# Kernel tuning notes

Measured on AMD Instinct MI355X. Metric: run time of the kernel, lower is better.

## Reference

```python
import jax, jax.numpy as jnp
import numpy as np

N = 400000       # maxvar(100000) * batch_size(4) nodes
E = 6400000      # edges, avg degree 16
D_IN, H, OUT = 1, 128, 2
N_MP = 4         # num_layers - 1 message-passing layers


def _bn(x, g, b):
    # BatchNorm1d in training mode: biased variance over the node/batch dim
    m = jnp.mean(x, axis=0)
    v = jnp.var(x, axis=0)
    return (x - m) * jax.lax.rsqrt(v + 1e-5) * g + b


def _gin_layer(h, src, dst, eps_l, W1, b1, g1, bb1, W2, b2, og, ob):
    # pooled = A @ h  (unweighted sparse adjacency) + (1+eps)*h
    pooled = jax.ops.segment_sum(h[src], dst, num_segments=N)
    pooled = pooled + (1.0 + eps_l) * h
    # 2-layer MLP (Linear -> BN -> ReLU -> Linear), then outer BN + ReLU
    x = jax.nn.relu(_bn(pooled @ W1 + b1, g1, bb1))
    x = x @ W2 + b2
    return jax.nn.relu(_bn(x, og, ob))


def setup_inputs() -> dict:
    key = jax.random.key(0)
    ks = jax.random.split(key, 10)
    f32 = jnp.float32
    inp = {
        "batch_size": 4,
        "var_feat": jax.random.normal(ks[0], (N, D_IN), f32),
        "edge_src": jax.random.randint(ks[1], (E,), 0, N, jnp.int32),
        "edge_dst": jax.random.randint(ks[2], (E,), 0, N, jnp.int32),
        "eps": jnp.ones((N_MP,), f32),
        # layer 0 MLP: D_IN -> H -> H
        "mlp0_W1": jax.random.normal(ks[3], (D_IN, H), f32) * 0.1,
        "mlp0_b1": jnp.zeros((H,), f32),
        "mlp0_g1": jnp.ones((H,), f32),
        "mlp0_bb1": jnp.zeros((H,), f32),
        "mlp0_W2": jax.random.normal(ks[4], (H, H), f32) * 0.05,
        "mlp0_b2": jnp.zeros((H,), f32),
        "bn0_g": jnp.ones((H,), f32),
        "bn0_b": jnp.zeros((H,), f32),
        # layers 1..3 MLPs stacked: H -> H -> H
        "mlpW1": jax.random.normal(ks[5], (N_MP - 1, H, H), f32) * 0.05,
        "mlpb1": jnp.zeros((N_MP - 1, H), f32),
        "mlpg1": jnp.ones((N_MP - 1, H), f32),
        "mlpbb1": jnp.zeros((N_MP - 1, H), f32),
        "mlpW2": jax.random.normal(ks[6], (N_MP - 1, H, H), f32) * 0.05,
        "mlpb2": jnp.zeros((N_MP - 1, H), f32),
        "bn_g": jnp.ones((N_MP - 1, H), f32),
        "bn_b": jnp.zeros((N_MP - 1, H), f32),
        # final classifier fc1: H -> OUT
        "fc1_W": jax.random.normal(ks[7], (H, OUT), f32) * 0.05,
        "fc1_b": jnp.zeros((OUT,), f32),
    }
    return inp


def reference(batch_size, var_feat, edge_src, edge_dst, eps,
              mlp0_W1, mlp0_b1, mlp0_g1, mlp0_bb1, mlp0_W2, mlp0_b2,
              bn0_g, bn0_b,
              mlpW1, mlpb1, mlpg1, mlpbb1, mlpW2, mlpb2, bn_g, bn_b,
              fc1_W, fc1_b):
    del batch_size  # unused in the var.var / no-lfa path
    h = _gin_layer(var_feat, edge_src, edge_dst, eps[0],
                   mlp0_W1, mlp0_b1, mlp0_g1, mlp0_bb1, mlp0_W2, mlp0_b2,
                   bn0_g, bn0_b)
    for l in range(N_MP - 1):
        h = _gin_layer(h, edge_src, edge_dst, eps[l + 1],
                       mlpW1[l], mlpb1[l], mlpg1[l], mlpbb1[l],
                       mlpW2[l], mlpb2[l], bn_g[l], bn_b[l])
    # var_classification head
    return jax.nn.softmax(h @ fc1_W + fc1_b, axis=1)
```

## Files before the change

### kernel.cpp

```cpp
#include <hip/hip_runtime.h>
#include <math.h>

#define HD 128
#define LDP 136

typedef _Float16 f16;
typedef _Float16 f16x8 __attribute__((ext_vector_type(8)));
typedef float f32x4 __attribute__((ext_vector_type(4)));

static __device__ __forceinline__ float h2f(unsigned short s) {
    f16 v; __builtin_memcpy(&v, &s, 2); return (float)v;
}

__global__ void k_diag(float* __restrict__ out, int n, float val) {
    for (int i = blockIdx.x * blockDim.x + threadIdx.x; i < n; i += gridDim.x * blockDim.x)
        out[i] = val;
}

__global__ void k_zero(float* __restrict__ p, int n) {
    for (int i = threadIdx.x; i < n; i += blockDim.x) p[i] = 0.f;
}
__global__ void k_zeroi(int* __restrict__ p, int n) {
    for (int i = blockIdx.x * blockDim.x + threadIdx.x; i < n; i += gridDim.x * blockDim.x)
        p[i] = 0;
}
__global__ void k_copyi(const int* __restrict__ a, int* __restrict__ b, int n) {
    for (int i = blockIdx.x * blockDim.x + threadIdx.x; i < n; i += gridDim.x * blockDim.x)
        b[i] = a[i];
}

__global__ void k_hist(const int* __restrict__ dst, int* __restrict__ row_ptr, int e) {
    for (int i = blockIdx.x * blockDim.x + threadIdx.x; i < e; i += gridDim.x * blockDim.x)
        atomicAdd(&row_ptr[dst[i] + 1], 1);
}

#define SCAN_B 1024
__global__ void k_scan_block(int* __restrict__ a, int n, int* __restrict__ bsum) {
    __shared__ int s[SCAN_B];
    int base = blockIdx.x * SCAN_B;
    int i = base + threadIdx.x;
    int v = (i < n) ? a[i] : 0;
    s[threadIdx.x] = v;
    __syncthreads();
    for (int o = 1; o < SCAN_B; o <<= 1) {
        int t = (threadIdx.x >= o) ? s[threadIdx.x - o] : 0;
        __syncthreads();
        s[threadIdx.x] += t;
        __syncthreads();
    }
    if (i < n) a[i] = s[threadIdx.x];
    if (threadIdx.x == 0) bsum[blockIdx.x] = s[SCAN_B - 1];
}
__global__ void k_scan_serial(int* __restrict__ bsum, int nb) {
    int run = 0;
    for (int b = 0; b < nb; b++) { int t = bsum[b]; bsum[b] = run; run += t; }
}
__global__ void k_scan_add(int* __restrict__ a, int n, const int* __restrict__ bsum) {
    int base = blockIdx.x * SCAN_B;
    int i = base + threadIdx.x;
    if (i < n) a[i] += bsum[blockIdx.x];
}
__global__ void k_bucket(const int* __restrict__ src, const int* __restrict__ dst,
                         int* __restrict__ fill, int* __restrict__ src_sorted, int e) {
    for (int i = blockIdx.x * blockDim.x + threadIdx.x; i < e; i += gridDim.x * blockDim.x) {
        int pos = atomicAdd(&fill[dst[i]], 1);
        src_sorted[pos] = src[i];
    }
}

__global__ void k_pool0(const float* __restrict__ vf, const int* __restrict__ row_ptr,
                        const int* __restrict__ srcs, const float* __restrict__ eps,
                        float* __restrict__ p0, int n) {
    float ep = 1.f + eps[0];
    for (int i = blockIdx.x * blockDim.x + threadIdx.x; i < n; i += gridDim.x * blockDim.x) {
        float s = ep * vf[i];
        int j1 = row_ptr[i + 1];
        for (int j = row_ptr[i]; j < j1; j++) s += vf[srcs[j]];
        p0[i] = s;
    }
}

__global__ void k_p0_stats(const float* __restrict__ p0, float* __restrict__ stats, int n) {
    __shared__ float rs[256], rq[256];
    float s = 0.f, q = 0.f;
    for (int i = blockIdx.x * blockDim.x + threadIdx.x; i < n; i += gridDim.x * blockDim.x) {
        float v = p0[i]; s += v; q += v * v;
    }
    int t = threadIdx.x;
    rs[t] = s; rq[t] = q;
    __syncthreads();
    for (int o = 128; o > 0; o >>= 1) {
        if (t < o) { rs[t] += rs[t + o]; rq[t] += rq[t + o]; }
        __syncthreads();
    }
    if (t == 0) { unsafeAtomicAdd(&stats[0], rs[0]); unsafeAtomicAdd(&stats[1], rq[0]); }
}

__global__ void k_l0_prep(float* __restrict__ stats, const float* __restrict__ W1,
                          const float* __restrict__ g1, const float* __restrict__ bb1,
                          float* __restrict__ A0, float* __restrict__ Sh0, int n) {
    float mp = stats[0] / n;
    float vp = stats[1] / n - mp * mp;
    int c = threadIdx.x;
    float w = W1[c];
    A0[c] = w * rsqrtf(vp * w * w + 1e-5f) * g1[c];
    Sh0[c] = bb1[c];
    if (c == 0) stats[2] = mp;
}

static __device__ __forceinline__ void acc_aff(f16x8 v, const float* scv, const float* shv,
                                               float* a) {
#pragma unroll
    for (int j = 0; j < 8; j++)
        a[j] += fmaxf((float)v[j] * scv[j] + shv[j], 0.f);
}

__global__ __launch_bounds__(256) void k_pgemm(
    const f16* __restrict__ h, const int* __restrict__ row_ptr,
    const int* __restrict__ src_sorted, const float* __restrict__ eps, int li,
    const float* __restrict__ sc, const float* __restrict__ sh,
    const float* __restrict__ W, const float* __restrict__ bias,
    f16* __restrict__ out, float* __restrict__ gsum, float* __restrict__ gsq, int n) {
    __shared__ f16 Wl[HD * LDP];
    __shared__ f16 Pl[32 * LDP];
    const int t = threadIdx.x;
    const int lane = t & 63, w = t >> 6;
    const int l15 = lane & 15, lq = lane >> 4;

    for (int p = 0; p < 64; p++) {
        int idx = p * 256 + t;
        Wl[(idx & 127) * LDP + (idx >> 7)] = (f16)W[idx];
    }

    const int ga = t >> 4, ca = (t & 15) * 8;
    float scv[8], shv[8];
    *(float4*)&scv[0] = *(const float4*)&sc[ca];
    *(float4*)&scv[4] = *(const float4*)&sc[ca + 4];
    *(float4*)&shv[0] = *(const float4*)&sh[ca];
    *(float4*)&shv[4] = *(const float4*)&sh[ca + 4];
    const float ep = 1.f + eps[li];

    const int rt = (w & 1) * 16;
    const int ctb = (w >> 1) * 4;
    float bv[4];
#pragma unroll
    for (int i = 0; i < 4; i++) bv[i] = bias[(ctb + i) * 16 + l15];

    float s8[8] = {0}, q8[8] = {0};
    const int ntiles = n / 32;
    for (int tile = blockIdx.x; tile < ntiles; tile += gridDim.x) {
        __syncthreads();
#pragma unroll
        for (int rr = 0; rr < 2; rr++) {
            const int r = tile * 32 + ga * 2 + rr;
            float a[8];
            {
                f16x8 u = *(const f16x8*)&h[(size_t)r * HD + ca];
#pragma unroll
                for (int j = 0; j < 8; j++)
                    a[j] = ep * fmaxf((float)u[j] * scv[j] + shv[j], 0.f);
            }
            const int j0 = row_ptr[r], j1 = row_ptr[r + 1];
            int j = j0;
            for (; j + 3 < j1; j += 4) {
                int s0 = src_sorted[j], s1 = src_sorted[j + 1];
                int s2 = src_sorted[j + 2], s3 = src_sorted[j + 3];
                f16x8 v0 = *(const f16x8*)&h[(size_t)s0 * HD + ca];
                f16x8 v1 = *(const f16x8*)&h[(size_t)s1 * HD + ca];
                f16x8 v2 = *(const f16x8*)&h[(size_t)s2 * HD + ca];
                f16x8 v3 = *(const f16x8*)&h[(size_t)s3 * HD + ca];
                acc_aff(v0, scv, shv, a);
                acc_aff(v1, scv, shv, a);
                acc_aff(v2, scv, shv, a);
                acc_aff(v3, scv, shv, a);
            }
            for (; j < j1; j++) {
                f16x8 v = *(const f16x8*)&h[(size_t)src_sorted[j] * HD + ca];
                acc_aff(v, scv, shv, a);
            }
            f16x8 o;
#pragma unroll
            for (int jj = 0; jj < 8; jj++) o[jj] = (f16)a[jj];
            *(f16x8*)&Pl[(ga * 2 + rr) * LDP + ca] = o;
        }
        __syncthreads();
        f16x8 af[4];
#pragma unroll
        for (int k0 = 0; k0 < 4; k0++)
            af[k0] = *(const f16x8*)&Pl[(rt + l15) * LDP + k0 * 32 + 8 * lq];
        __syncthreads();
#pragma unroll
        for (int i = 0; i < 4; i++) {
            f32x4 acc = {0.f, 0.f, 0.f, 0.f};
            const int c0 = (ctb + i) * 16;
#pragma unroll
            for (int k0 = 0; k0 < 4; k0++) {
                f16x8 bf = *(const f16x8*)&Wl[(c0 + l15) * LDP + k0 * 32 + 8 * lq];
                acc = __builtin_amdgcn_mfma_f32_16x16x32_f16(af[k0], bf, acc, 0, 0, 0);
            }
#pragma unroll
            for (int ri = 0; ri < 4; ri++)
                Pl[(rt + lq * 4 + ri) * LDP + c0 + l15] = (f16)(acc[ri] + bv[i]);
        }
        __syncthreads();
#pragma unroll
        for (int p = 0; p < 2; p++) {
            int u = p * 256 + t;
            int row = u >> 4;
            f16x8 v = *(const f16x8*)&Pl[row * LDP + ca];
            *(f16x8*)&out[(size_t)(tile * 32 + row) * HD + ca] = v;
#pragma unroll
            for (int j = 0; j < 8; j++) {
                float f = (float)v[j];
                s8[j] += f; q8[j] += f * f;
            }
        }
    }

    __syncthreads();
    float* red = (float*)Wl;
#pragma unroll
    for (int j = 0; j < 8; j++) { red[t * 16 + j] = s8[j]; red[t * 16 + 8 + j] = q8[j]; }
    __syncthreads();
    if (t < HD) {
        int g = t >> 3, j = t & 7;
        float ts = 0.f, tq = 0.f;
#pragma unroll
        for (int i = 0; i < 16; i++) {
            ts += red[(i * 16 + g) * 16 + j];
            tq += red[(i * 16 + g) * 16 + 8 + j];
        }
        unsafeAtomicAdd(&gsum[t], ts);
        unsafeAtomicAdd(&gsq[t], tq);
    }
}

template <int MODE>
__global__ __launch_bounds__(256) void k_gemm(
    const void* __restrict__ in_, const float* __restrict__ W,
    const float* __restrict__ bias,
    const float* __restrict__ tsc, const float* __restrict__ tsh,
    const float* __restrict__ mstat,
    f16* __restrict__ out, float* __restrict__ gsum, float* __restrict__ gsq, int n) {
    __shared__ f16 Wl[HD * LDP];
    __shared__ f16 Al[64 * LDP];
    const int t = threadIdx.x;
    const int lane = t & 63, w = t >> 6;
    const int l15 = lane & 15, lq = lane >> 4;

    for (int p = 0; p < 64; p++) {
        int idx = p * 256 + t;
        Wl[(idx & 127) * LDP + (idx >> 7)] = (f16)W[idx];
    }

    const int ca = (t & 15) * 8;
    float tscv[8], tshv[8];
    *(float4*)&tscv[0] = *(const float4*)&tsc[ca];
    *(float4*)&tscv[4] = *(const float4*)&tsc[ca + 4];
    *(float4*)&tshv[0] = *(const float4*)&tsh[ca];
    *(float4*)&tshv[4] = *(const float4*)&tsh[ca + 4];
    float mp = 0.f;
    if (MODE == 2) mp = mstat[2];
    float bv[8];
#pragma unroll
    for (int ct = 0; ct < 8; ct++) bv[ct] = bias[ct * 16 + l15];

    const int r0 = w * 16;
    float s8[8] = {0}, q8[8] = {0};
    const int ntiles = n / 64;
    for (int tile = blockIdx.x; tile < ntiles; tile += gridDim.x) {
        __syncthreads();
#pragma unroll
        for (int p = 0; p < 4; p++) {
            const int row = (t >> 4) + p * 16;
            const int grow = tile * 64 + row;
            f16x8 o;
            if (MODE == 1) {
                f16x8 zv = *(const f16x8*)&((const f16*)in_)[(size_t)grow * HD + ca];
#pragma unroll
                for (int j = 0; j < 8; j++)
                    o[j] = (f16)fmaxf((float)zv[j] * tscv[j] + tshv[j], 0.f);
            } else {
                const float pr = ((const float*)in_)[grow] - mp;
#pragma unroll
                for (int j = 0; j < 8; j++)
                    o[j] = (f16)fmaxf(pr * tscv[j] + tshv[j], 0.f);
            }
            *(f16x8*)&Al[row * LDP + ca] = o;
        }
        __syncthreads();
        f16x8 af[4];
#pragma unroll
        for (int k0 = 0; k0 < 4; k0++)
            af[k0] = *(const f16x8*)&Al[(r0 + l15) * LDP + k0 * 32 + 8 * lq];
#pragma unroll
        for (int ct = 0; ct < 8; ct++) {
            f32x4 acc = {0.f, 0.f, 0.f, 0.f};
#pragma unroll
            for (int k0 = 0; k0 < 4; k0++) {
                f16x8 bf = *(const f16x8*)&Wl[(ct * 16 + l15) * LDP + k0 * 32 + 8 * lq];
                acc = __builtin_amdgcn_mfma_f32_16x16x32_f16(af[k0], bf, acc, 0, 0, 0);
            }
#pragma unroll
            for (int ri = 0; ri < 4; ri++)
                Al[(r0 + lq * 4 + ri) * LDP + ct * 16 + l15] = (f16)(acc[ri] + bv[ct]);
        }
        __syncthreads();
#pragma unroll
        for (int p = 0; p < 4; p++) {
            int row = (t >> 4) + p * 16;
            f16x8 v = *(const f16x8*)&Al[row * LDP + ca];
            *(f16x8*)&out[(size_t)(tile * 64 + row) * HD + ca] = v;
#pragma unroll
            for (int j = 0; j < 8; j++) {
                float f = (float)v[j];
                s8[j] += f; q8[j] += f * f;
            }
        }
    }

    __syncthreads();
    float* red = (float*)Al;
#pragma unroll
    for (int j = 0; j < 8; j++) { red[t * 16 + j] = s8[j]; red[t * 16 + 8 + j] = q8[j]; }
    __syncthreads();
    if (t < HD) {
        int g = t >> 3, j = t & 7;
        float ts = 0.f, tq = 0.f;
#pragma unroll
        for (int i = 0; i < 16; i++) {
            ts += red[(i * 16 + g) * 16 + j];
            tq += red[(i * 16 + g) * 16 + 8 + j];
        }
        unsafeAtomicAdd(&gsum[t], ts);
        unsafeAtomicAdd(&gsq[t], tq);
    }
}

__global__ void k_finalize(const float* __restrict__ gsum, const float* __restrict__ gsq,
                           const float* __restrict__ g, const float* __restrict__ b,
                           float* __restrict__ sc, float* __restrict__ sh, int n) {
    int c = threadIdx.x;
    float m = gsum[c] / n;
    float v = gsq[c] / n - m * m;
    float s = rsqrtf(v + 1e-5f) * g[c];
    sc[c] = s;
    sh[c] = b[c] - m * s;
}

__global__ void k_head(const unsigned short* __restrict__ z, const float* __restrict__ sc,
                       const float* __restrict__ sh, const float* __restrict__ fw,
                       const float* __restrict__ fb, float* __restrict__ out, int n) {
    int gid  = blockIdx.x * blockDim.x + threadIdx.x;
    int lane = threadIdx.x & 63;
    int w    = gid >> 6;
    int nw   = (gridDim.x * blockDim.x) >> 6;
    int c    = lane * 2;
    float s0 = sc[c], s1 = sc[c + 1], t0 = sh[c], t1 = sh[c + 1];
    float w00 = fw[c * 2], w01 = fw[c * 2 + 1], w10 = fw[c * 2 + 2], w11 = fw[c * 2 + 3];
    float fb0 = fb[0], fb1 = fb[1];
    for (int r = w; r < n; r += nw) {
        unsigned int u = *(const unsigned int*)&z[(size_t)r * HD + c];
        float zx = h2f((unsigned short)(u & 0xffffu));
        float zy = h2f((unsigned short)(u >> 16));
        float x0 = fmaxf(zx * s0 + t0, 0.f);
        float x1 = fmaxf(zy * s1 + t1, 0.f);
        float l0 = x0 * w00 + x1 * w10;
        float l1 = x0 * w01 + x1 * w11;
#pragma unroll
        for (int o = 32; o > 0; o >>= 1) {
            l0 += __shfl_xor(l0, o, 64);
            l1 += __shfl_xor(l1, o, 64);
        }
        if (lane == 0) {
            l0 += fb0; l1 += fb1;
            float m  = fmaxf(l0, l1);
            float e0 = expf(l0 - m), e1 = expf(l1 - m);
            float inv = 1.f / (e0 + e1);
            *(float2*)&out[(size_t)r * 2] = make_float2(e0 * inv, e1 * inv);
        }
    }
}

extern "C" void kernel_launch(void* const* d_in, const int* in_sizes, int n_in,
                              void* d_out, int out_size, void* d_ws, size_t ws_size,
                              hipStream_t stream) {
    const float* vf    = (const float*)d_in[1];
    const int*   src   = (const int*)d_in[2];
    const int*   dst   = (const int*)d_in[3];
    const float* eps   = (const float*)d_in[4];
    const float* W1_0  = (const float*)d_in[5];
    const float* g1_0  = (const float*)d_in[7];
    const float* bb1_0 = (const float*)d_in[8];
    const float* W2_0  = (const float*)d_in[9];
    const float* b2_0  = (const float*)d_in[10];
    const float* bn0g  = (const float*)d_in[11];
    const float* bn0b  = (const float*)d_in[12];
    const float* W1s   = (const float*)d_in[13];
    const float* b1s   = (const float*)d_in[14];
    const float* g1s   = (const float*)d_in[15];
    const float* bb1s  = (const float*)d_in[16];
    const float* W2s   = (const float*)d_in[17];
    const float* b2s   = (const float*)d_in[18];
    const float* bngs  = (const float*)d_in[19];
    const float* bnbs  = (const float*)d_in[20];
    const float* fw    = (const float*)d_in[21];
    const float* fb    = (const float*)d_in[22];
    float* out = (float*)d_out;

    const int N = in_sizes[1];
    const int E = in_sizes[2];

    const size_t needed = (size_t)N * HD * 2 * 2 + (size_t)(N + 8 + 9 * 128 + 512) * 4
                        + (size_t)(2 * N + 1 + E) * 4;
    if (ws_size < needed) {
        float code = (float)(double)(ws_size >> 20);
        k_diag<<<2048, 256, 0, stream>>>(out, out_size, code);
        return;
    }

    f16* H            = (f16*)d_ws;
    f16* Z            = H + (size_t)N * HD;
    float* p0         = (float*)(Z + (size_t)N * HD);
    float* stats      = p0 + N;
    float* gsum       = stats + 8;
    float* gsq        = gsum + HD;
    float* sc1        = gsq + HD;
    float* sh1        = sc1 + HD;
    float* sc2        = sh1 + HD;
    float* sh2        = sc2 + HD;
    float* A0         = sh2 + HD;
    float* Sh0        = A0 + HD;
    int* bsum         = (int*)(Sh0 + HD);
    int* row_ptr      = bsum + 512;
    int* fill         = row_ptr + (N + 1);
    int* src_sorted   = fill + N;

    const int n1 = N + 1;
    const int nsb = (n1 + SCAN_B - 1) / SCAN_B;
    k_zeroi<<<512, 256, 0, stream>>>(row_ptr, n1);
    k_hist<<<4096, 256, 0, stream>>>(dst, row_ptr, E);
    k_scan_block<<<nsb, SCAN_B, 0, stream>>>(row_ptr, n1, bsum);
    k_scan_serial<<<1, 1, 0, stream>>>(bsum, nsb);
    k_scan_add<<<nsb, SCAN_B, 0, stream>>>(row_ptr, n1, bsum);
    k_copyi<<<512, 256, 0, stream>>>(row_ptr, fill, N);
    k_bucket<<<4096, 256, 0, stream>>>(src, dst, fill, src_sorted, E);

    k_pool0<<<2048, 256, 0, stream>>>(vf, row_ptr, src_sorted, eps, p0, N);
    k_zero<<<1, 256, 0, stream>>>(stats, 8);
    k_p0_stats<<<1024, 256, 0, stream>>>(p0, stats, N);
    k_l0_prep<<<1, 128, 0, stream>>>(stats, W1_0, g1_0, bb1_0, A0, Sh0, N);
    k_zero<<<1, 256, 0, stream>>>(gsum, 2 * HD);
    k_gemm<2><<<2048, 256, 0, stream>>>(p0, W2_0, b2_0, A0, Sh0, stats, H, gsum, gsq, N);
    k_finalize<<<1, 128, 0, stream>>>(gsum, gsq, bn0g, bn0b, sc2, sh2, N);

    for (int l = 0; l < 3; l++) {
        k_zero<<<1, 256, 0, stream>>>(gsum, 2 * HD);
        k_pgemm<<<2048, 256, 0, stream>>>(H, row_ptr, src_sorted, eps, l + 1, sc2, sh2,
                                          W1s + (size_t)l * HD * HD, b1s + l * HD,
                                          Z, gsum, gsq, N);
        k_finalize<<<1, 128, 0, stream>>>(gsum, gsq, g1s + l * HD, bb1s + l * HD, sc1, sh1, N);
        k_zero<<<1, 256, 0, stream>>>(gsum, 2 * HD);
        k_gemm<1><<<2048, 256, 0, stream>>>(Z, W2s + (size_t)l * HD * HD, b2s + l * HD,
                                            sc1, sh1, nullptr, H, gsum, gsq, N);
        k_finalize<<<1, 128, 0, stream>>>(gsum, gsq, bngs + l * HD, bnbs + l * HD, sc2, sh2, N);
    }

    k_head<<<4096, 256, 0, stream>>>((const unsigned short*)H, sc2, sh2, fw, fb, out, N);
}
```

Before: 2.148 ms.

## Pre-apply BN+ReLU in place before gather, and chunk edge bucketing by dst range

Adds an in-place elementwise pass that applies the previous layer's BN affine and ReLU to the fp16 node features once, so the pgemm gather loop only sums raw neighbor rows instead of redoing the affine+ReLU per edge. Separately, the edge bucketing scatter is split into four passes over the full edge list, each handling only destinations in one quarter of the node range, to localize atomic and scatter writes in cache. The trade-off is an extra full read/write of the feature matrix per layer and four full reads of the edge arrays. Activations are now rounded to fp16 after ReLU before aggregation, which slightly changes precision.

```diff
diff --git a/kernel.cpp b/kernel.cpp
--- a/kernel.cpp
+++ b/kernel.cpp
@@ -3,6 +3,7 @@
 
 #define HD 128
 #define LDP 136
+#define NBCH 4
 
 typedef _Float16 f16;
 typedef _Float16 f16x8 __attribute__((ext_vector_type(8)));
@@ -60,11 +61,17 @@
     int i = base + threadIdx.x;
     if (i < n) a[i] += bsum[blockIdx.x];
 }
-__global__ void k_bucket(const int* __restrict__ src, const int* __restrict__ dst,
-                         int* __restrict__ fill, int* __restrict__ src_sorted, int e) {
+
+__global__ void k_bucket_chunk(const int* __restrict__ src, const int* __restrict__ dst,
+                               int* __restrict__ fill, int* __restrict__ src_sorted,
+                               int e, int base, int nc) {
     for (int i = blockIdx.x * blockDim.x + threadIdx.x; i < e; i += gridDim.x * blockDim.x) {
-        int pos = atomicAdd(&fill[dst[i]], 1);
-        src_sorted[pos] = src[i];
+        int d = dst[i];
+        unsigned int rel = (unsigned int)(d - base);
+        if (rel < (unsigned int)nc) {
+            int pos = atomicAdd(&fill[d], 1);
+            src_sorted[pos] = src[i];
+        }
     }
 }
 
@@ -108,17 +115,35 @@
     if (c == 0) stats[2] = mp;
 }
 
-static __device__ __forceinline__ void acc_aff(f16x8 v, const float* scv, const float* shv,
-                                               float* a) {
-#pragma unroll
-    for (int j = 0; j < 8; j++)
-        a[j] += fmaxf((float)v[j] * scv[j] + shv[j], 0.f);
+__global__ void k_prep_ip(f16* __restrict__ hz, const float* __restrict__ sc,
+                          const float* __restrict__ sh, int n8) {
+    for (int i = blockIdx.x * blockDim.x + threadIdx.x; i < n8; i += gridDim.x * blockDim.x) {
+        int c0 = (i & 15) * 8;
+        f16x8 v = *(const f16x8*)&hz[(size_t)i * 8];
+        float4 s0 = *(const float4*)&sc[c0];
+        float4 s1 = *(const float4*)&sc[c0 + 4];
+        float4 h0 = *(const float4*)&sh[c0];
+        float4 h1 = *(const float4*)&sh[c0 + 4];
+        v[0] = (f16)fmaxf((float)v[0] * s0.x + h0.x, 0.f);
+        v[1] = (f16)fmaxf((float)v[1] * s0.y + h0.y, 0.f);
+        v[2] = (f16)fmaxf((float)v[2] * s0.z + h0.z, 0.f);
+        v[3] = (f16)fmaxf((float)v[3] * s0.w + h0.w, 0.f);
+        v[4] = (f16)fmaxf((float)v[4] * s1.x + h1.x, 0.f);
+        v[5] = (f16)fmaxf((float)v[5] * s1.y + h1.y, 0.f);
+        v[6] = (f16)fmaxf((float)v[6] * s1.z + h1.z, 0.f);
+        v[7] = (f16)fmaxf((float)v[7] * s1.w + h1.w, 0.f);
+        *(f16x8*)&hz[(size_t)i * 8] = v;
+    }
+}
+
+static __device__ __forceinline__ void acc_sum(f16x8 v, float* a) {
+#pragma unroll
+    for (int j = 0; j < 8; j++) a[j] += (float)v[j];
 }
 
 __global__ __launch_bounds__(256) void k_pgemm(
     const f16* __restrict__ h, const int* __restrict__ row_ptr,
     const int* __restrict__ src_sorted, const float* __restrict__ eps, int li,
-    const float* __restrict__ sc, const float* __restrict__ sh,
     const float* __restrict__ W, const float* __restrict__ bias,
     f16* __restrict__ out, float* __restrict__ gsum, float* __restrict__ gsq, int n) {
     __shared__ f16 Wl[HD * LDP];
@@ -133,11 +158,6 @@
     }
 
     const int ga = t >> 4, ca = (t & 15) * 8;
-    float scv[8], shv[8];
-    *(float4*)&scv[0] = *(const float4*)&sc[ca];
-    *(float4*)&scv[4] = *(const float4*)&sc[ca + 4];
-    *(float4*)&shv[0] = *(const float4*)&sh[ca];
-    *(float4*)&shv[4] = *(const float4*)&sh[ca + 4];
     const float ep = 1.f + eps[li];
 
     const int rt = (w & 1) * 16;
@@ -157,8 +177,7 @@
             {
                 f16x8 u = *(const f16x8*)&h[(size_t)r * HD + ca];
 #pragma unroll
-                for (int j = 0; j < 8; j++)
-                    a[j] = ep * fmaxf((float)u[j] * scv[j] + shv[j], 0.f);
+                for (int j = 0; j < 8; j++) a[j] = ep * (float)u[j];
             }
             const int j0 = row_ptr[r], j1 = row_ptr[r + 1];
             int j = j0;
@@ -169,14 +188,11 @@
                 f16x8 v1 = *(const f16x8*)&h[(size_t)s1 * HD + ca];
                 f16x8 v2 = *(const f16x8*)&h[(size_t)s2 * HD + ca];
                 f16x8 v3 = *(const f16x8*)&h[(size_t)s3 * HD + ca];
-                acc_aff(v0, scv, shv, a);
-                acc_aff(v1, scv, shv, a);
-                acc_aff(v2, scv, shv, a);
-                acc_aff(v3, scv, shv, a);
+                acc_sum(v0, a); acc_sum(v1, a); acc_sum(v2, a); acc_sum(v3, a);
             }
             for (; j < j1; j++) {
                 f16x8 v = *(const f16x8*)&h[(size_t)src_sorted[j] * HD + ca];
-                acc_aff(v, scv, shv, a);
+                acc_sum(v, a);
             }
             f16x8 o;
 #pragma unroll
@@ -444,7 +460,12 @@
     k_scan_serial<<<1, 1, 0, stream>>>(bsum, nsb);
     k_scan_add<<<nsb, SCAN_B, 0, stream>>>(row_ptr, n1, bsum);
     k_copyi<<<512, 256, 0, stream>>>(row_ptr, fill, N);
-    k_bucket<<<4096, 256, 0, stream>>>(src, dst, fill, src_sorted, E);
+    {
+        const int NC2 = N / NBCH;
+        for (int c = 0; c < NBCH; c++)
+            k_bucket_chunk<<<4096, 256, 0, stream>>>(src, dst, fill, src_sorted,
+                                                     E, c * NC2, NC2);
+    }
 
     k_pool0<<<2048, 256, 0, stream>>>(vf, row_ptr, src_sorted, eps, p0, N);
     k_zero<<<1, 256, 0, stream>>>(stats, 8);
@@ -455,8 +476,9 @@
     k_finalize<<<1, 128, 0, stream>>>(gsum, gsq, bn0g, bn0b, sc2, sh2, N);
 
     for (int l = 0; l < 3; l++) {
+        k_prep_ip<<<4096, 256, 0, stream>>>(H, sc2, sh2, N * (HD / 8));
         k_zero<<<1, 256, 0, stream>>>(gsum, 2 * HD);
-        k_pgemm<<<2048, 256, 0, stream>>>(H, row_ptr, src_sorted, eps, l + 1, sc2, sh2,
+        k_pgemm<<<2048, 256, 0, stream>>>(H, row_ptr, src_sorted, eps, l + 1,
                                           W1s + (size_t)l * HD * HD, b1s + l * HD,
                                           Z, gsum, gsq, N);
         k_finalize<<<1, 128, 0, stream>>>(gsum, gsq, g1s + l * HD, bb1s + l * HD, sc1, sh1, N);
```

New measurement: 2.265 ms. 1.05x slower.
